# Kernel optimization log

Hardware: AMD Instinct MI355X
Metric: run time of the kernel (lower is better)

Reference implementation:

```python
import jax, jax.numpy as jnp
import numpy as np

EMBED_DIM = 1024
NUM_HEADS = 16
HEAD_DIM = EMBED_DIM // NUM_HEADS
LN_EPS = 1e-5


def setup_inputs() -> dict:
    key = jax.random.key(0)
    ks = jax.random.split(key, 5)
    N, L, C = 32, 577, EMBED_DIM
    x = jax.random.normal(ks[0], (N, L, C), dtype=jnp.float32)
    ln1_g = jnp.ones((C,), dtype=jnp.float32)
    ln1_b = jnp.zeros((C,), dtype=jnp.float32)
    w_in = jax.random.normal(ks[1], (3 * C, C), dtype=jnp.float32) * (C ** -0.5)
    b_in = jax.random.normal(ks[2], (3 * C,), dtype=jnp.float32) * 0.02
    w_out = jax.random.normal(ks[3], (C, C), dtype=jnp.float32) * (C ** -0.5)
    b_out = jax.random.normal(ks[4], (C,), dtype=jnp.float32) * 0.02
    return {"x": x, "ln1_g": ln1_g, "ln1_b": ln1_b, "w_in": w_in,
            "b_in": b_in, "w_out": w_out, "b_out": b_out}


def _layernorm(x, g, b):
    mu = jnp.mean(x, axis=-1, keepdims=True)
    var = jnp.mean(jnp.square(x - mu), axis=-1, keepdims=True)
    return (x - mu) * jax.lax.rsqrt(var + LN_EPS) * g + b


def reference(x, ln1_g, ln1_b, w_in, b_in, w_out, b_out):
    # ClearCLIP last block, attn_variant='qq', keep_residual=False, keep_ffn=False.
    N, L, C = x.shape
    H, D = NUM_HEADS, HEAD_DIM
    z = _layernorm(x, ln1_g, ln1_b)
    qkv = z @ w_in.T + b_in                      # (N, L, 3C)
    q, k, v = jnp.split(qkv, 3, axis=-1)
    k = q                                        # 'qq' self-self variant
    def heads(t):
        return t.reshape(N, L, H, D).transpose(0, 2, 1, 3)  # (N, H, L, D)
    q, k, v = heads(q), heads(k), heads(v)
    scale = 1.0 / np.sqrt(D).astype(np.float32)
    scores = jnp.einsum('nhld,nhsd->nhls', q, k) * scale    # (N, H, L, L)
    attn = jax.nn.softmax(scores, axis=-1)
    out = jnp.einsum('nhls,nhsd->nhld', attn, v)            # (N, H, L, D)
    out = out.transpose(0, 2, 1, 3).reshape(N, L, C)
    return out @ w_out.T + b_out                 # ls_1 = Identity, no residual/FFN
```

## Files before the change

kernel.cpp:

```cpp
#include <hip/hip_runtime.h>
#include <stdint.h>

typedef short bf16x8 __attribute__((ext_vector_type(8)));
typedef float f32x4 __attribute__((ext_vector_type(4)));
typedef unsigned int uint4v __attribute__((ext_vector_type(4)));
typedef unsigned short ushort4v __attribute__((ext_vector_type(4)));
typedef float float4v __attribute__((ext_vector_type(4)));

#define MROWS 18464
#define SEQ   577
#define CDIM  1024
#define SPAD  640
#define W1ELEMS (2048*1024)
#define W2ELEMS (1024*1024)
#define SQC 0.42466089f

__device__ __forceinline__ unsigned short f2bf(float f) {
  unsigned int u = __float_as_uint(f);
  u += 0x7fffu + ((u >> 16) & 1u);
  return (unsigned short)(u >> 16);
}

__device__ __forceinline__ void load_lds16(const void* g, void* lds) {
  __builtin_amdgcn_global_load_lds(
      (const __attribute__((address_space(1))) unsigned int*)(uint64_t)(uintptr_t)g,
      (__attribute__((address_space(3))) unsigned int*)(unsigned int)(uintptr_t)lds,
      16, 0, 0);
}

__global__ __launch_bounds__(256) void ln_kernel(const float* __restrict__ x,
                                                 const float* __restrict__ g,
                                                 const float* __restrict__ b,
                                                 unsigned short* __restrict__ z) {
  const int row = blockIdx.x;
  const int t = threadIdx.x;
  const float4v v = *(const float4v*)(x + (size_t)row * CDIM + t * 4);
  float s  = v[0] + v[1] + v[2] + v[3];
  float ss = v[0]*v[0] + v[1]*v[1] + v[2]*v[2] + v[3]*v[3];
  #pragma unroll
  for (int off = 1; off < 64; off <<= 1) { s += __shfl_xor(s, off); ss += __shfl_xor(ss, off); }
  __shared__ float rs[4], rss[4];
  const int w = t >> 6, l = t & 63;
  if (l == 0) { rs[w] = s; rss[w] = ss; }
  __syncthreads();
  s = rs[0] + rs[1] + rs[2] + rs[3];
  ss = rss[0] + rss[1] + rss[2] + rss[3];
  const float mu = s * (1.0f / CDIM);
  const float var = ss * (1.0f / CDIM) - mu * mu;
  const float rstd = rsqrtf(var + 1e-5f);
  const float4v gv = *(const float4v*)(g + t * 4);
  const float4v bv = *(const float4v*)(b + t * 4);
  ushort4v o;
  #pragma unroll
  for (int j = 0; j < 4; ++j) o[j] = f2bf((v[j] - mu) * rstd * gv[j] + bv[j]);
  *(ushort4v*)(z + (size_t)row * CDIM + t * 4) = o;
}

__global__ __launch_bounds__(256) void conv_kernel(const float* __restrict__ w_in,
                                                   const float* __restrict__ w_out,
                                                   unsigned short* __restrict__ wqv,
                                                   unsigned short* __restrict__ wo,
                                                   unsigned short* __restrict__ vt) {
  const int idx = blockIdx.x * 256 + threadIdx.x;
  const int e = idx * 4;
  if (e < W1ELEMS) {
    const int row = e >> 10;
    const int srow = row < 1024 ? row : row + 1024;
    const float4v v = *(const float4v*)(w_in + (size_t)srow * 1024 + (e & 1023));
    ushort4v o;
    #pragma unroll
    for (int j = 0; j < 4; ++j) o[j] = f2bf(v[j]);
    *(ushort4v*)(wqv + e) = o;
  } else if (e < W1ELEMS + W2ELEMS) {
    const int e2 = e - W1ELEMS;
    const float4v v = *(const float4v*)(w_out + e2);
    ushort4v o;
    #pragma unroll
    for (int j = 0; j < 4; ++j) o[j] = f2bf(v[j]);
    *(ushort4v*)(wo + e2) = o;
  } else {
    const int pidx = idx - (W1ELEMS + W2ELEMS) / 4;
    const int ic = pidx >> 3, part = pidx & 7;
    *(uint4v*)(vt + (size_t)ic * SPAD + 576 + part * 8) = (uint4v)0u;
  }
}

template<int MODE>
__global__ __launch_bounds__(1024, 4) void gemm256(const unsigned short* __restrict__ A,
                                                   const unsigned short* __restrict__ B,
                                                   const float* __restrict__ bias,
                                                   void* __restrict__ outp,
                                                   unsigned short* __restrict__ vtout) {
  __shared__ char smem[65536];
  const int t = threadIdx.x;
  const int w = t >> 6, l = t & 63;
  int p, c;
  if constexpr (MODE == 0) {
    const int L = (blockIdx.x & 7) * 73 + (blockIdx.x >> 3);
    p = L >> 3; c = L & 7;
  } else {
    const int xcd = blockIdx.x & 7, j0 = blockIdx.x >> 3;
    const int L = (xcd < 4 ? xcd * 37 : 148 + (xcd - 4) * 36) + j0;
    p = L >> 2; c = L & 3;
  }
  const int m0 = p * 256, n0 = c * 256;
  const int wm = w >> 2, wn = w & 3;
  const int g4 = (l >> 4) * 4;
  const int fr = l & 15;
  const int g = l >> 4;
  const int rswz = ((fr >> 1) & 3) << 4;

  f32x4 acc[4][4];
  #pragma unroll
  for (int i = 0; i < 4; ++i)
    #pragma unroll
    for (int j = 0; j < 4; ++j) acc[i][j] = (f32x4)0.0f;

  const int dchunk = ((l & 3) ^ ((l >> 3) & 3)) * 8;
  int ra = m0 + w * 16 + (l >> 2); if (ra > MROWS - 1) ra = MROWS - 1;
  const unsigned short* pA = A + (size_t)ra * 1024 + dchunk;
  const unsigned short* pB = B + (size_t)(n0 + w * 16 + (l >> 2)) * 1024 + dchunk;
  const int ldst = w * 1024 + l * 16;

  #define STG(kt, slot)                                    \
    {                                                      \
      char* const d_ = smem + (slot) * 32768 + ldst;       \
      load_lds16(pA + (kt) * 32, d_);                      \
      load_lds16(pB + (kt) * 32, d_ + 16384);              \
    }

  STG(0, 0)
  __syncthreads();

  for (int kb = 0; kb < 32; ++kb) {
    const int b = kb & 1;
    if (kb < 31) STG(kb + 1, b ^ 1)
    const char* Ab = smem + b * 32768;
    const char* Bb = Ab + 16384;
    bf16x8 af[4], bf[4];
    #pragma unroll
    for (int i = 0; i < 4; ++i)
      af[i] = *(const bf16x8*)(Ab + (wm * 64 + i * 16 + fr) * 64 + ((g * 16) ^ rswz));
    #pragma unroll
    for (int j = 0; j < 4; ++j)
      bf[j] = *(const bf16x8*)(Bb + (wn * 64 + j * 16 + fr) * 64 + ((g * 16) ^ rswz));
    #pragma unroll
    for (int i = 0; i < 4; ++i)
      #pragma unroll
      for (int j = 0; j < 4; ++j)
        acc[i][j] = __builtin_amdgcn_mfma_f32_16x16x32_bf16(af[i], bf[j], acc[i][j], 0, 0, 0);
    __syncthreads();
  }
  #undef STG

  if constexpr (MODE == 0) {
    unsigned short* sm = (unsigned short*)smem;
    const bool isq = (n0 < 1024);
    const float* bb = isq ? (bias + n0) : (bias + 1024 + n0);
    const float scl = isq ? SQC : 1.0f;
    float bcol[4];
    #pragma unroll
    for (int j = 0; j < 4; ++j) bcol[j] = bb[wn * 64 + j * 16 + fr];
    for (int pass = 0; pass < 4; ++pass) {
      if (wm == pass) {
        #pragma unroll
        for (int i = 0; i < 4; ++i)
          #pragma unroll
          for (int j = 0; j < 4; ++j)
            #pragma unroll
            for (int r = 0; r < 4; ++r)
              sm[(i * 16 + g4 + r) * 264 + wn * 64 + j * 16 + fr] =
                  f2bf((acc[i][j][r] + bcol[j]) * scl);
      }
      __syncthreads();
      if (isq) {
        unsigned short* o = (unsigned short*)outp;
        #pragma unroll
        for (int it = 0; it < 2; ++it) {
          const int cid = it * 1024 + t;
          const int row = cid >> 5, ch = cid & 31;
          const int grow = m0 + pass * 64 + row;
          if (grow < MROWS)
            *(uint4v*)(o + (size_t)grow * 1024 + n0 + ch * 8) =
                *(const uint4v*)(sm + row * 264 + ch * 8);
        }
      } else {
        const int tokloc = t & 63, chgrp = t >> 6;
        const int token = m0 + pass * 64 + tokloc;
        if (token < MROWS) {
          const unsigned int nimg = (unsigned int)token / 577u;
          const int s = token - (int)(nimg * 577u);
          unsigned short* op =
              vtout + ((size_t)nimg * 1024 + (n0 - 1024) + chgrp * 16) * SPAD + s;
          const unsigned short* sp = sm + tokloc * 264 + chgrp * 16;
          #pragma unroll 8
          for (int it = 0; it < 16; ++it)
            op[(size_t)it * SPAD] = sp[it];
        }
      }
      __syncthreads();
    }
  } else {
    float* smf = (float*)smem;
    float bcol[4];
    #pragma unroll
    for (int j = 0; j < 4; ++j) bcol[j] = bias[n0 + wn * 64 + j * 16 + fr];
    float* o = (float*)outp;
    for (int q8 = 0; q8 < 8; ++q8) {
      if (wm == (q8 >> 1)) {
        const int i0 = (q8 & 1) * 2;
        #pragma unroll
        for (int i2 = 0; i2 < 2; ++i2)
          #pragma unroll
          for (int j = 0; j < 4; ++j)
            #pragma unroll
            for (int r = 0; r < 4; ++r)
              smf[(i2 * 16 + g4 + r) * 260 + wn * 64 + j * 16 + fr] =
                  acc[i0 + i2][j][r] + bcol[j];
      }
      __syncthreads();
      #pragma unroll
      for (int it = 0; it < 2; ++it) {
        const int cid = it * 1024 + t;
        const int row = cid >> 6, ch = cid & 63;
        const int grow = m0 + q8 * 32 + row;
        if (grow < MROWS)
          *(float4v*)(o + (size_t)grow * 1024 + n0 + ch * 4) =
              *(const float4v*)(smf + row * 260 + ch * 4);
      }
      __syncthreads();
    }
  }
}

__global__ __launch_bounds__(256) void attn_kernel(const unsigned short* __restrict__ qbuf,
                                                   const unsigned short* __restrict__ vt,
                                                   unsigned short* __restrict__ out) {
  __shared__ char smem[32768];
  const int t = threadIdx.x, w = t >> 6, l = t & 63;
  const int g = l >> 4, fr = l & 15;
  const int bid = blockIdx.x;
  const int xcd = bid & 7, idx = bid >> 3;
  const int nhl = idx / 5;
  const int qb = idx - nhl * 5;
  const int nh = xcd * 64 + nhl;
  const int n = nh >> 4, h = nh & 15;
  const size_t rowbase = (size_t)n * SEQ;
  const int sw = (l & 7) << 4;

  bf16x8 bq[2][2];
  #pragma unroll
  for (int half = 0; half < 2; ++half) {
    const unsigned short* qp =
        qbuf + (rowbase + qb * 128 + half * 64 + w * 16 + fr) * 1024 + h * 64 + g * 8;
    bq[half][0] = *(const bf16x8*)qp;
    bq[half][1] = *(const bf16x8*)(qp + 32);
  }

  const int srow = l >> 3;
  const int scolE = ((((l & 7) * 16) ^ ((srow & 7) << 4)) >> 1);
  const unsigned short* ksrc = qbuf + (rowbase + w * 16 + srow) * 1024 + h * 64 + scolE;
  const unsigned short* vsrc = vt + ((size_t)nh * 64 + w * 16 + srow) * SPAD + scolE;

  f32x4 acc[2][4];
  #pragma unroll
  for (int half = 0; half < 2; ++half)
    #pragma unroll
    for (int cf = 0; cf < 4; ++cf) acc[half][cf] = (f32x4)0.0f;
  float l_run[2] = {0.0f, 0.0f};

  {
    char* kdst = smem + (w * 16) * 128;
    char* vdst = smem + 8192 + (w * 16) * 128;
    load_lds16(ksrc, kdst);
    load_lds16(ksrc + (size_t)8 * 1024, kdst + 1024);
    load_lds16(vsrc, vdst);
    load_lds16(vsrc + 8 * SPAD, vdst + 1024);
  }
  __syncthreads();

  for (int kb = 0; kb < 10; ++kb) {
    const int b = kb & 1;
    const char* kbuf = smem + b * 16384;
    const char* vbuf = kbuf + 8192;

    if (kb < 9) {
      char* kdst = smem + (b ^ 1) * 16384 + (w * 16) * 128;
      char* vdst = kdst + 8192;
      load_lds16(ksrc + (size_t)((kb + 1) * 64) * 1024, kdst);
      load_lds16(ksrc + (size_t)((kb + 1) * 64 + 8) * 1024, kdst + 1024);
      load_lds16(vsrc + (kb + 1) * 64, vdst);
      load_lds16(vsrc + 8 * SPAD + (kb + 1) * 64, vdst + 1024);
    }

    f32x4 s4[2][4];
    #pragma unroll
    for (int half = 0; half < 2; ++half)
      #pragma unroll
      for (int cf = 0; cf < 4; ++cf) s4[half][cf] = (f32x4)0.0f;
    #pragma unroll
    for (int kk = 0; kk < 2; ++kk)
      #pragma unroll
      for (int cf = 0; cf < 4; ++cf) {
        const bf16x8 af = *(const bf16x8*)(kbuf + (cf * 16 + fr) * 128 + ((kk * 64 + g * 16) ^ sw));
        s4[0][cf] = __builtin_amdgcn_mfma_f32_16x16x32_bf16(af, bq[0][kk], s4[0][cf], 0, 0, 0);
        s4[1][cf] = __builtin_amdgcn_mfma_f32_16x16x32_bf16(af, bq[1][kk], s4[1][cf], 0, 0, 0);
      }

    if (kb == 9) {
      #pragma unroll
      for (int half = 0; half < 2; ++half) {
        #pragma unroll
        for (int cf = 0; cf < 4; ++cf)
          #pragma unroll
          for (int r = 0; r < 4; ++r)
            if (cf != 0 || r != 0) s4[half][cf][r] = -__builtin_inff();
        s4[half][0][0] = (g == 0) ? s4[half][0][0] : -__builtin_inff();
      }
    }

    bf16x8 ap[2][2];
    #pragma unroll
    for (int half = 0; half < 2; ++half) {
      float sum = 0.0f;
      #pragma unroll
      for (int cf = 0; cf < 4; ++cf)
        #pragma unroll
        for (int r = 0; r < 4; ++r) {
          const float p2 = __builtin_amdgcn_exp2f(s4[half][cf][r]);
          s4[half][cf][r] = p2;
          sum += p2;
        }
      sum += __shfl_xor(sum, 16);
      sum += __shfl_xor(sum, 32);
      l_run[half] += sum;

      unsigned int pka[4], pkb[4];
      #pragma unroll
      for (int cf = 0; cf < 4; ++cf) {
        asm("v_cvt_pk_bf16_f32 %0, %1, %2" : "=v"(pka[cf]) : "v"(s4[half][cf][0]), "v"(s4[half][cf][1]));
        asm("v_cvt_pk_bf16_f32 %0, %1, %2" : "=v"(pkb[cf]) : "v"(s4[half][cf][2]), "v"(s4[half][cf][3]));
      }
      #pragma unroll
      for (int kk = 0; kk < 2; ++kk) {
        unsigned int a0 = pka[2 * kk], b0 = pka[2 * kk + 1];
        unsigned int a1 = pkb[2 * kk], b1 = pkb[2 * kk + 1];
        asm("v_permlane32_swap_b32 %0, %1" : "+v"(a0), "+v"(b0));
        asm("v_permlane16_swap_b32 %0, %1" : "+v"(a0), "+v"(b0));
        asm("v_permlane32_swap_b32 %0, %1" : "+v"(a1), "+v"(b1));
        asm("v_permlane16_swap_b32 %0, %1" : "+v"(a1), "+v"(b1));
        union { unsigned int i[4]; bf16x8 v; } u;
        u.i[0] = a0; u.i[1] = a1; u.i[2] = b0; u.i[3] = b1;
        ap[half][kk] = u.v;
      }
    }

    #pragma unroll
    for (int kk = 0; kk < 2; ++kk)
      #pragma unroll
      for (int cf = 0; cf < 4; ++cf) {
        const bf16x8 bv = *(const bf16x8*)(vbuf + (cf * 16 + fr) * 128 + ((kk * 64 + g * 16) ^ sw));
        acc[0][cf] = __builtin_amdgcn_mfma_f32_16x16x32_bf16(ap[0][kk], bv, acc[0][cf], 0, 0, 0);
        acc[1][cf] = __builtin_amdgcn_mfma_f32_16x16x32_bf16(ap[1][kk], bv, acc[1][cf], 0, 0, 0);
      }

    __syncthreads();
  }

  #pragma unroll
  for (int half = 0; half < 2; ++half) {
    const float rcp = 1.0f / l_run[half];
    #pragma unroll
    for (int r = 0; r < 4; ++r) {
      const float rr = __shfl(rcp, g * 4 + r);
      const int qg = qb * 128 + half * 64 + w * 16 + g * 4 + r;
      if (qg < SEQ) {
        #pragma unroll
        for (int cf = 0; cf < 4; ++cf)
          out[(rowbase + qg) * 1024 + h * 64 + cf * 16 + fr] = f2bf(acc[half][cf][r] * rr);
      }
    }
  }
}

extern "C" void kernel_launch(void* const* d_in, const int* in_sizes, int n_in,
                              void* d_out, int out_size, void* d_ws, size_t ws_size,
                              hipStream_t stream) {
  const float* x     = (const float*)d_in[0];
  const float* ln_g  = (const float*)d_in[1];
  const float* ln_b  = (const float*)d_in[2];
  const float* w_in  = (const float*)d_in[3];
  const float* b_in  = (const float*)d_in[4];
  const float* w_out = (const float*)d_in[5];
  const float* b_out = (const float*)d_in[6];

  unsigned short* z    = (unsigned short*)d_ws;
  unsigned short* qbuf = z + (size_t)MROWS * 1024;
  unsigned short* vt   = qbuf + (size_t)MROWS * 1024;
  unsigned short* wqv  = vt + (size_t)512 * 64 * SPAD;
  unsigned short* wo   = wqv + (size_t)2048 * 1024;

  ln_kernel<<<MROWS, 256, 0, stream>>>(x, ln_g, ln_b, z);
  conv_kernel<<<4096, 256, 0, stream>>>(w_in, w_out, wqv, wo, vt);
  gemm256<0><<<584, 1024, 0, stream>>>(z, wqv, b_in, qbuf, vt);
  attn_kernel<<<2560, 256, 0, stream>>>(qbuf, vt, z);
  gemm256<1><<<292, 1024, 0, stream>>>(z, wo, b_out, d_out, nullptr);
}
```

Baseline: 262.1 us.

## Load B operand directly to registers and double K tile in GEMM loop

The GEMM main loop now stages only the A tile through LDS, with 64-wide K tiles and a new XOR swizzle. Each wave loads its B fragments straight from global memory into registers and double-buffers them across the two K halves. Iterations are halved and the loop synchronizes with explicit vmcnt waits and sched barriers. This is meant to cut LDS traffic and barrier count. In exchange it raises register pressure and makes B global loads uncoalesced per-lane 16-byte reads that are repeated by each wm wave.

Measured after the change: 447.9 us. 70.9% more time.

```diff
diff --git a/kernel.cpp b/kernel.cpp
--- a/kernel.cpp
+++ b/kernel.cpp
@@ -108,7 +108,8 @@
   const int g4 = (l >> 4) * 4;
   const int fr = l & 15;
   const int g = l >> 4;
-  const int rswz = ((fr >> 1) & 3) << 4;
+  const int fb = g * 16;
+  const int sw = (l & 7) << 4;
 
   f32x4 acc[4][4];
   #pragma unroll
@@ -116,42 +117,68 @@
     #pragma unroll
     for (int j = 0; j < 4; ++j) acc[i][j] = (f32x4)0.0f;
 
-  const int dchunk = ((l & 3) ^ ((l >> 3) & 3)) * 8;
-  int ra = m0 + w * 16 + (l >> 2); if (ra > MROWS - 1) ra = MROWS - 1;
-  const unsigned short* pA = A + (size_t)ra * 1024 + dchunk;
-  const unsigned short* pB = B + (size_t)(n0 + w * 16 + (l >> 2)) * 1024 + dchunk;
-  const int ldst = w * 1024 + l * 16;
-
-  #define STG(kt, slot)                                    \
+  const int srow = l >> 3;
+  const int scol = ((((l & 7) * 16) ^ ((srow & 7) << 4)) >> 1);
+  int ra0 = m0 + w * 16 + srow;     if (ra0 > MROWS - 1) ra0 = MROWS - 1;
+  int ra1 = m0 + w * 16 + 8 + srow; if (ra1 > MROWS - 1) ra1 = MROWS - 1;
+  const unsigned short* pA0 = A + (size_t)ra0 * 1024 + scol;
+  const unsigned short* pA1 = A + (size_t)ra1 * 1024 + scol;
+
+  #define STGA(kt, slot)                                   \
     {                                                      \
-      char* const d_ = smem + (slot) * 32768 + ldst;       \
-      load_lds16(pA + (kt) * 32, d_);                      \
-      load_lds16(pB + (kt) * 32, d_ + 16384);              \
-    }
-
-  STG(0, 0)
+      char* const d_ = smem + (slot) * 32768 + w * 2048;   \
+      load_lds16(pA0 + (kt) * 64, d_);                     \
+      load_lds16(pA1 + (kt) * 64, d_ + 1024);              \
+    }
+
+  const unsigned short* pB[4];
+  #pragma unroll
+  for (int j = 0; j < 4; ++j)
+    pB[j] = B + (size_t)(n0 + wn * 64 + j * 16 + fr) * 1024 + g * 8;
+  bf16x8 bA[4], bB[4];
+
+  STGA(0, 0)
+  __builtin_amdgcn_sched_barrier(0);
+  #pragma unroll
+  for (int j = 0; j < 4; ++j) { bA[j] = *(const bf16x8*)(pB[j]); bB[j] = *(const bf16x8*)(pB[j] + 32); }
+  asm volatile("s_waitcnt vmcnt(0)" ::: "memory");
+  __builtin_amdgcn_s_barrier();
+  __builtin_amdgcn_sched_barrier(0);
+
+  for (int kb = 0; kb < 16; ++kb) {
+    const int slot = kb & 1;
+    const char* Ab = smem + slot * 32768;
+    if (kb < 15) STGA(kb + 1, slot ^ 1)
+    __builtin_amdgcn_sched_barrier(0);
+    #pragma unroll
+    for (int i = 0; i < 4; ++i) {
+      const bf16x8 af = *(const bf16x8*)(Ab + (wm * 64 + i * 16 + fr) * 128 + (fb ^ sw));
+      #pragma unroll
+      for (int j = 0; j < 4; ++j)
+        acc[i][j] = __builtin_amdgcn_mfma_f32_16x16x32_bf16(af, bA[j], acc[i][j], 0, 0, 0);
+    }
+    if (kb < 15) {
+      #pragma unroll
+      for (int j = 0; j < 4; ++j) bA[j] = *(const bf16x8*)(pB[j] + 64);
+    }
+    #pragma unroll
+    for (int i = 0; i < 4; ++i) {
+      const bf16x8 af = *(const bf16x8*)(Ab + (wm * 64 + i * 16 + fr) * 128 + ((64 + fb) ^ sw));
+      #pragma unroll
+      for (int j = 0; j < 4; ++j)
+        acc[i][j] = __builtin_amdgcn_mfma_f32_16x16x32_bf16(af, bB[j], acc[i][j], 0, 0, 0);
+    }
+    if (kb < 15) {
+      #pragma unroll
+      for (int j = 0; j < 4; ++j) { bB[j] = *(const bf16x8*)(pB[j] + 96); pB[j] += 64; }
+    }
+    asm volatile("s_waitcnt vmcnt(8)" ::: "memory");
+    __builtin_amdgcn_sched_barrier(0);
+    __builtin_amdgcn_s_barrier();
+    __builtin_amdgcn_sched_barrier(0);
+  }
+  #undef STGA
   __syncthreads();
-
-  for (int kb = 0; kb < 32; ++kb) {
-    const int b = kb & 1;
-    if (kb < 31) STG(kb + 1, b ^ 1)
-    const char* Ab = smem + b * 32768;
-    const char* Bb = Ab + 16384;
-    bf16x8 af[4], bf[4];
-    #pragma unroll
-    for (int i = 0; i < 4; ++i)
-      af[i] = *(const bf16x8*)(Ab + (wm * 64 + i * 16 + fr) * 64 + ((g * 16) ^ rswz));
-    #pragma unroll
-    for (int j = 0; j < 4; ++j)
-      bf[j] = *(const bf16x8*)(Bb + (wn * 64 + j * 16 + fr) * 64 + ((g * 16) ^ rswz));
-    #pragma unroll
-    for (int i = 0; i < 4; ++i)
-      #pragma unroll
-      for (int j = 0; j < 4; ++j)
-        acc[i][j] = __builtin_amdgcn_mfma_f32_16x16x32_bf16(af[i], bf[j], acc[i][j], 0, 0, 0);
-    __syncthreads();
-  }
-  #undef STG
 
   if constexpr (MODE == 0) {
     unsigned short* sm = (unsigned short*)smem;
```
